# Kernel tuning notes

Measured on AMD Instinct MI355X. Metric: run time of the kernel, lower is better.

Reference implementation:

```python
import jax, jax.numpy as jnp
import numpy as np

B, N, M, D, H, F = 2, 2048, 2048, 512, 8, 2048
EPS = 1e-6


def _ln(x, g, b):
    mu = x.mean(-1, keepdims=True)
    var = ((x - mu) ** 2).mean(-1, keepdims=True)
    return (x - mu) / jnp.sqrt(var + EPS) * g + b


def setup_inputs() -> dict:
    key = jax.random.key(0)
    ks = jax.random.split(key, 12)
    g = lambda k, s: (jax.random.normal(k, s, jnp.float32) * 0.02)
    inp = {
        "x": jax.random.normal(ks[0], (B, N, D), jnp.float32),
        "y": jax.random.normal(ks[1], (B, M, D), jnp.float32),
        "mask_x": jnp.ones((B, N), jnp.float32),
        "mask_y": jnp.ones((B, M), jnp.float32),
        # MaskAttention params (weights stored as [in, out], applied as x @ W + b)
        "Wq": g(ks[2], (D, D)), "bq": jnp.zeros((D,), jnp.float32),
        "Wk": g(ks[3], (D, D)), "bk": jnp.zeros((D,), jnp.float32),
        "Wv": g(ks[4], (D, D)), "bv": jnp.zeros((D,), jnp.float32),
        "Wo": g(ks[5], (D, D)), "bo": jnp.zeros((D,), jnp.float32),
        # Mlp params
        "W1": g(ks[6], (D, F)), "b1": g(ks[7], (F,)) * 1e-4,
        "W2": g(ks[8], (F, D)), "b2": g(ks[9], (D,)) * 1e-4,
        # LayerNorm params (attention_norm shared between x and y; ffn_norm)
        "ln1_g": jnp.ones((D,), jnp.float32), "ln1_b": jnp.zeros((D,), jnp.float32),
        "ln2_g": jnp.ones((D,), jnp.float32), "ln2_b": jnp.zeros((D,), jnp.float32),
    }
    return inp


def reference(x, y, mask_x, mask_y, Wq, bq, Wk, bk, Wv, bv, Wo, bo,
              W1, b1, W2, b2, ln1_g, ln1_b, ln2_g, ln2_b):
    b, n, d = x.shape
    dh = d // H
    h = x
    xn = _ln(x, ln1_g, ln1_b)   # shared attention_norm
    yn = _ln(y, ln1_g, ln1_b)
    # masked Q/K/V projections (mask applied to mixed layers before head split)
    q = (xn @ Wq + bq) * mask_x[..., None]
    k = (yn @ Wk + bk) * mask_y[..., None]
    v = (yn @ Wv + bv) * mask_y[..., None]
    q = q.reshape(b, n, H, dh)
    k = k.reshape(b, -1, H, dh)
    v = v.reshape(b, -1, H, dh)
    scores = jnp.einsum("bnhd,bmhd->bhnm", q, k) / np.sqrt(dh)  # [B,H,N,M]
    probs = jax.nn.softmax(scores, axis=-1)
    ctx = jnp.einsum("bhnm,bmhd->bnhd", probs, v).reshape(b, n, d)
    attn_out = ctx @ Wo + bo  # proj_dropout is identity in eval
    x = h + attn_out
    h2 = x
    xn2 = _ln(x, ln2_g, ln2_b)
    ff = jax.nn.gelu(xn2 @ W1 + b1, approximate=False) @ W2 + b2
    return h2 + ff
```

## Files before the change

kernel.cpp:

```cpp
#include <hip/hip_runtime.h>
#include <hip/hip_bf16.h>

#define B_  2
#define N_  2048
#define M_  2048
#define D_  512
#define H_  8
#define F_  2048
#define DH_ 64
#define ROWS 4096

#define SPLIT 2
#define KV_PER (M_ / SPLIT)
#define NT (KV_PER / 64)
#define ATT_GRID (16 * 16 * SPLIT)

typedef __bf16 bf16x8 __attribute__((ext_vector_type(8)));
typedef __bf16 bf16x4v __attribute__((ext_vector_type(4)));
typedef float  f32x4  __attribute__((ext_vector_type(4)));
using bf16 = __hip_bfloat16;

__global__ __launch_bounds__(256) void ln_kernel(
    const float* __restrict__ in, const float* __restrict__ gam,
    const float* __restrict__ bet, bf16* __restrict__ out)
{
    int wave = threadIdx.x >> 6, lane = threadIdx.x & 63;
    int row  = blockIdx.x * 4 + wave;
    const float* p = in + (size_t)row * D_ + lane * 8;
    float4 v0 = *(const float4*)p;
    float4 v1 = *(const float4*)(p + 4);
    float s  = v0.x + v0.y + v0.z + v0.w + v1.x + v1.y + v1.z + v1.w;
    float ss = v0.x*v0.x + v0.y*v0.y + v0.z*v0.z + v0.w*v0.w
             + v1.x*v1.x + v1.y*v1.y + v1.z*v1.z + v1.w*v1.w;
    for (int m = 1; m < 64; m <<= 1) {
        s  += __shfl_xor(s,  m, 64);
        ss += __shfl_xor(ss, m, 64);
    }
    float mu   = s * (1.f / D_);
    float var  = ss * (1.f / D_) - mu * mu;
    float rstd = rsqrtf(var + 1e-6f);
    int c = lane * 8;
    float4 g0 = *(const float4*)(gam + c), g1 = *(const float4*)(gam + c + 4);
    float4 b0 = *(const float4*)(bet + c), b1 = *(const float4*)(bet + c + 4);
    bf16* o = out + (size_t)row * D_ + c;
    o[0] = __float2bfloat16((v0.x - mu) * rstd * g0.x + b0.x);
    o[1] = __float2bfloat16((v0.y - mu) * rstd * g0.y + b0.y);
    o[2] = __float2bfloat16((v0.z - mu) * rstd * g0.z + b0.z);
    o[3] = __float2bfloat16((v0.w - mu) * rstd * g0.w + b0.w);
    o[4] = __float2bfloat16((v1.x - mu) * rstd * g1.x + b1.x);
    o[5] = __float2bfloat16((v1.y - mu) * rstd * g1.y + b1.y);
    o[6] = __float2bfloat16((v1.z - mu) * rstd * g1.z + b1.z);
    o[7] = __float2bfloat16((v1.w - mu) * rstd * g1.w + b1.w);
}

__global__ void wtrans_kernel(const float* __restrict__ W, bf16* __restrict__ Wt,
                              int K, int N)
{
    __shared__ float t[32][33];
    int tx = threadIdx.x, ty = threadIdx.y;
    int n0 = blockIdx.x * 32, k0 = blockIdx.y * 32;
    for (int j = 0; j < 32; j += 8)
        t[ty + j][tx] = W[(size_t)(k0 + ty + j) * N + n0 + tx];
    __syncthreads();
    for (int j = 0; j < 32; j += 8)
        Wt[(size_t)(n0 + ty + j) * K + k0 + tx] = __float2bfloat16(t[tx][ty + j]);
}

__global__ void wtrans4_kernel(const float* __restrict__ Wq, const float* __restrict__ Wk,
                               const float* __restrict__ Wv, const float* __restrict__ Wo,
                               bf16* __restrict__ Wqt, bf16* __restrict__ Wkt,
                               bf16* __restrict__ Wvt, bf16* __restrict__ Wot)
{
    int z = blockIdx.z;
    const float* W = z == 0 ? Wq : (z == 1 ? Wk : (z == 2 ? Wv : Wo));
    bf16* Wt       = z == 0 ? Wqt : (z == 1 ? Wkt : (z == 2 ? Wvt : Wot));
    __shared__ float t[32][33];
    int tx = threadIdx.x, ty = threadIdx.y;
    int n0 = blockIdx.x * 32, k0 = blockIdx.y * 32;
    for (int j = 0; j < 32; j += 8)
        t[ty + j][tx] = W[(size_t)(k0 + ty + j) * D_ + n0 + tx];
    __syncthreads();
    for (int j = 0; j < 32; j += 8)
        Wt[(size_t)(n0 + ty + j) * D_ + k0 + tx] = __float2bfloat16(t[tx][ty + j]);
}

__global__ void vtrans_kernel(const bf16* __restrict__ v, bf16* __restrict__ vt)
{
    __shared__ bf16 t[32][33];
    int tx = threadIdx.x, ty = threadIdx.y;
    int bh = blockIdx.z, b = bh >> 3, h = bh & 7;
    int m0 = blockIdx.x * 32, d0 = blockIdx.y * 32;
    for (int j = 0; j < 32; j += 8)
        t[ty + j][tx] = v[(size_t)(b * M_ + m0 + ty + j) * D_ + h * DH_ + d0 + tx];
    __syncthreads();
    for (int j = 0; j < 32; j += 8)
        vt[((size_t)bh * DH_ + d0 + ty + j) * M_ + m0 + tx] = t[tx][ty + j];
}

#define BM 128
#define BN 128
#define BK 32
#define LDK 40

#define GEMM_BODY(Aptr, Btptr, KK, EPILOGUE)                                         \
    __shared__ bf16 As[BM * LDK];                                                    \
    __shared__ bf16 Bs[BN * LDK];                                                    \
    int t = threadIdx.x;                                                             \
    int lane = t & 63, wave = t >> 6;                                                \
    int wm = wave >> 1, wn = wave & 1;                                               \
    int r16 = lane & 15, g = lane >> 4;                                              \
    int m0 = blockIdx.x * BM, n0 = blockIdx.y * BN;                                  \
    f32x4 acc[4][4] = {};                                                            \
    for (int k0 = 0; k0 < (KK); k0 += BK) {                                          \
        __syncthreads();                                                             \
        for (int it = 0; it < 2; ++it) {                                             \
            int c = it * 256 + t;                                                    \
            int row = c >> 2, ko = (c & 3) * 8;                                      \
            uint4 dA = *(const uint4*)((Aptr)  + (size_t)(m0 + row) * (KK) + k0 + ko); \
            *(uint4*)((char*)As + row * (LDK * 2) + ko * 2) = dA;                    \
            uint4 dB = *(const uint4*)((Btptr) + (size_t)(n0 + row) * (KK) + k0 + ko); \
            *(uint4*)((char*)Bs + row * (LDK * 2) + ko * 2) = dB;                    \
        }                                                                            \
        __syncthreads();                                                             \
        bf16x8 af[4], bfr[4];                                                        \
        for (int i = 0; i < 4; ++i)                                                  \
            af[i]  = *(const bf16x8*)((char*)As + (wm * 64 + i * 16 + r16) * (LDK * 2) + g * 16); \
        for (int i = 0; i < 4; ++i)                                                  \
            bfr[i] = *(const bf16x8*)((char*)Bs + (wn * 64 + i * 16 + r16) * (LDK * 2) + g * 16); \
        for (int i = 0; i < 4; ++i)                                                  \
            for (int j = 0; j < 4; ++j)                                              \
                acc[i][j] = __builtin_amdgcn_mfma_f32_16x16x32_bf16(af[i], bfr[j], acc[i][j], 0, 0, 0); \
    }                                                                                \
    for (int i = 0; i < 4; ++i) {                                                    \
        int rb = m0 + wm * 64 + i * 16 + g * 4;                                      \
        for (int j = 0; j < 4; ++j) {                                                \
            int cb = n0 + wn * 64 + j * 16 + r16;                                    \
            float bia = bias[cb];                                                    \
            for (int e = 0; e < 4; ++e) {                                            \
                int rr = rb + e;                                                     \
                float val = acc[i][j][e] + bia;                                      \
                EPILOGUE                                                             \
            }                                                                        \
        }                                                                            \
    }

template<bool GELU, bool RESID, bool ROWMASK, bool OUTBF>
__global__ __launch_bounds__(256) void gemm_bt(
    const bf16* __restrict__ A, const bf16* __restrict__ Bt,
    const float* __restrict__ bias, const float* __restrict__ resid,
    const float* __restrict__ rowmask,
    bf16* __restrict__ outb, float* __restrict__ outf,
    int Mr, int Nn, int K)
{
    GEMM_BODY(A, Bt, K,
        if (GELU)    val = 0.5f * val * (1.f + erff(val * 0.70710678118654752f));
        if (RESID)   val += resid[(size_t)rr * Nn + cb];
        if (ROWMASK) val *= rowmask[rr];
        if (OUTBF)   outb[(size_t)rr * Nn + cb] = __float2bfloat16(val);
        else         outf[(size_t)rr * Nn + cb] = val;
    )
}

template<bool RESID, bool ROWMASK, bool OUTBF>
__device__ __forceinline__ void gemm64_body(
    const bf16* __restrict__ A, const bf16* __restrict__ Bt,
    const float* __restrict__ bias, const float* __restrict__ resid,
    const float* __restrict__ rowmask,
    bf16* __restrict__ outb, float* __restrict__ outf,
    int Nn, int K)
{
    __shared__ __align__(16) char As[2][64 * 128];
    __shared__ __align__(16) char Bs[2][64 * 128];
    int t = threadIdx.x, lane = t & 63, wave = t >> 6;
    int wm = wave >> 1, wn = wave & 1;
    int r16 = lane & 15, g = lane >> 4;
    int m0 = blockIdx.x * 64, n0 = blockIdx.y * 64;

    const int sr0 = t >> 3, sr1 = sr0 + 32, sc = t & 7;
    const int wof0 = sr0 * 128 + ((sc ^ (sr0 & 7)) << 4);
    const int wof1 = sr1 * 128 + ((sc ^ (sr1 & 7)) << 4);
    const int rsw0 = ((g     ^ (r16 & 7)) << 4);
    const int rsw1 = (((4 + g) ^ (r16 & 7)) << 4);

    uint4 a0, a1, b0, b1;
#define G64_LOAD(k0)                                                         \
    a0 = *(const uint4*)(A  + (size_t)(m0 + sr0) * K + (k0) + sc * 8);       \
    a1 = *(const uint4*)(A  + (size_t)(m0 + sr1) * K + (k0) + sc * 8);       \
    b0 = *(const uint4*)(Bt + (size_t)(n0 + sr0) * K + (k0) + sc * 8);       \
    b1 = *(const uint4*)(Bt + (size_t)(n0 + sr1) * K + (k0) + sc * 8);
#define G64_WRITE(buf)                                                       \
    *(uint4*)(As[buf] + wof0) = a0;  *(uint4*)(As[buf] + wof1) = a1;         \
    *(uint4*)(Bs[buf] + wof0) = b0;  *(uint4*)(Bs[buf] + wof1) = b1;

    f32x4 acc[2][2] = {};
    G64_LOAD(0)
    G64_WRITE(0)
    int cur = 0;
    const int nit = K >> 6;
    for (int it = 0; it < nit; ++it) {
        if (it + 1 < nit) { G64_LOAD((it + 1) << 6) }
        __syncthreads();
        bf16x8 af[2][2], bfr[2][2];
#pragma unroll
        for (int i = 0; i < 2; ++i) {
            af[i][0] = *(const bf16x8*)(As[cur] + (wm * 32 + i * 16 + r16) * 128 + rsw0);
            af[i][1] = *(const bf16x8*)(As[cur] + (wm * 32 + i * 16 + r16) * 128 + rsw1);
            bfr[i][0] = *(const bf16x8*)(Bs[cur] + (wn * 32 + i * 16 + r16) * 128 + rsw0);
            bfr[i][1] = *(const bf16x8*)(Bs[cur] + (wn * 32 + i * 16 + r16) * 128 + rsw1);
        }
        __builtin_amdgcn_s_setprio(1);
#pragma unroll
        for (int i = 0; i < 2; ++i)
#pragma unroll
            for (int j = 0; j < 2; ++j) {
                acc[i][j] = __builtin_amdgcn_mfma_f32_16x16x32_bf16(af[i][0], bfr[j][0], acc[i][j], 0, 0, 0);
                acc[i][j] = __builtin_amdgcn_mfma_f32_16x16x32_bf16(af[i][1], bfr[j][1], acc[i][j], 0, 0, 0);
            }
        __builtin_amdgcn_s_setprio(0);
        if (it + 1 < nit) { G64_WRITE(cur ^ 1) }
        cur ^= 1;
    }
#undef G64_LOAD
#undef G64_WRITE

#pragma unroll
    for (int i = 0; i < 2; ++i) {
        int rb = m0 + wm * 32 + i * 16 + g * 4;
#pragma unroll
        for (int j = 0; j < 2; ++j) {
            int cb = n0 + wn * 32 + j * 16 + r16;
            float bia = bias[cb];
#pragma unroll
            for (int e = 0; e < 4; ++e) {
                int rr = rb + e;
                float val = acc[i][j][e] + bia;
                if (RESID)   val += resid[(size_t)rr * Nn + cb];
                if (ROWMASK) val *= rowmask[rr];
                if (OUTBF)   outb[(size_t)rr * Nn + cb] = __float2bfloat16(val);
                else         outf[(size_t)rr * Nn + cb] = val;
            }
        }
    }
}

template<bool RESID, bool OUTBF>
__global__ __launch_bounds__(256) void gemm64(
    const bf16* __restrict__ A, const bf16* __restrict__ Bt,
    const float* __restrict__ bias, const float* __restrict__ resid,
    bf16* __restrict__ outb, float* __restrict__ outf, int Nn, int K)
{
    gemm64_body<RESID, false, OUTBF>(A, Bt, bias, resid, nullptr, outb, outf, Nn, K);
}

__global__ __launch_bounds__(256) void gemm64_qkv(
    const bf16* __restrict__ xn, const bf16* __restrict__ yn,
    const bf16* __restrict__ Wqt, const bf16* __restrict__ Wkt, const bf16* __restrict__ Wvt,
    const float* __restrict__ bq, const float* __restrict__ bk, const float* __restrict__ bv,
    const float* __restrict__ mask_x, const float* __restrict__ mask_y,
    bf16* __restrict__ qb, bf16* __restrict__ kb, bf16* __restrict__ vb)
{
    int z = blockIdx.z;
    const bf16* A        = z == 0 ? xn : yn;
    const bf16* Bt       = z == 0 ? Wqt : (z == 1 ? Wkt : Wvt);
    const float* bias    = z == 0 ? bq  : (z == 1 ? bk  : bv);
    const float* rowmask = z == 0 ? mask_x : mask_y;
    bf16* outb           = z == 0 ? qb  : (z == 1 ? kb  : vb);
    gemm64_body<false, true, true>(A, Bt, bias, nullptr, rowmask, outb, nullptr, D_, D_);
}

__global__ __launch_bounds__(256, 3) void attn_kernel(
    const bf16* __restrict__ q, const bf16* __restrict__ kk,
    const bf16* __restrict__ vt, bf16* __restrict__ num,
    float* __restrict__ ml)
{
    int bid = blockIdx.x;
    int wg  = (bid & 7) * (ATT_GRID / 8) + (bid >> 3);
    int n0  = (wg & 15) * 128;
    int bh  = (wg >> 4) & 15;
    int sp  = wg >> 8;
    int b = bh >> 3, h = bh & 7;
    int t = threadIdx.x, lane = t & 63, wave = t >> 6;
    int ql = lane & 15, gg = lane >> 4;

    __shared__ __align__(16) char KsB[2][64 * 128];
    __shared__ __align__(16) char VsB[2][64 * 128];
    __shared__ __align__(16) bf16 plds[4][16][72];

    bf16x8 qf0[2], qf1[2];
    {
        int qr0 = b * N_ + n0 + wave * 32 + ql;
        for (int ks = 0; ks < 2; ++ks) {
            bf16x8 qv = *(const bf16x8*)(q + (size_t)qr0 * D_ + h * DH_ + ks * 32 + gg * 8);
            for (int j = 0; j < 8; ++j) qv[j] = (__bf16)((float)qv[j] * 0.125f);
            qf0[ks] = qv;
            bf16x8 qw = *(const bf16x8*)(q + (size_t)(qr0 + 16) * D_ + h * DH_ + ks * 32 + gg * 8);
            for (int j = 0; j < 8; ++j) qw[j] = (__bf16)((float)qw[j] * 0.125f);
            qf1[ks] = qw;
        }
    }

    f32x4 cacc0[4] = {}, cacc1[4] = {};
    float m0r = -1e30f, l0r = 0.f, m1r = -1e30f, l1r = 0.f;

    const bf16* kbase = kk + (size_t)(b * M_ + sp * KV_PER) * D_ + h * DH_;
    const bf16* vtb   = vt + (size_t)bh * DH_ * M_ + sp * KV_PER;

    const int k0r = t >> 3,          kc0 = t & 7;
    const int k1r = (t >> 3) + 32;
    const int wofs0 = k0r * 128 + ((kc0 ^ (k0r & 7)) << 4);
    const int wofs1 = k1r * 128 + ((kc0 ^ (k1r & 7)) << 4);
    const int rsw0 = ((gg     ^ (ql & 7)) << 4);
    const int rsw1 = (((4 + gg) ^ (ql & 7)) << 4);

#define STAGE_LOAD(tt)                                                              \
    kw0 = *(const uint4*)(kbase + (size_t)((tt) * 64 + k0r) * D_ + kc0 * 8);        \
    kw1 = *(const uint4*)(kbase + (size_t)((tt) * 64 + k1r) * D_ + kc0 * 8);        \
    vw0 = *(const uint4*)(vtb + (size_t)k0r * M_ + (tt) * 64 + kc0 * 8);            \
    vw1 = *(const uint4*)(vtb + (size_t)k1r * M_ + (tt) * 64 + kc0 * 8);

#define STAGE_WRITE(buf)                                                            \
    *(uint4*)(KsB[buf] + wofs0) = kw0;                                              \
    *(uint4*)(KsB[buf] + wofs1) = kw1;                                              \
    *(uint4*)(VsB[buf] + wofs0) = vw0;                                              \
    *(uint4*)(VsB[buf] + wofs1) = vw1;

#define SOFTMAX_PV(S, MR, LR, CACC)                                                 \
    {                                                                               \
        float tmax = fmaxf(                                                         \
            fmaxf(fmaxf(fmaxf(S[0][0], S[0][1]), fmaxf(S[0][2], S[0][3])),          \
                  fmaxf(fmaxf(S[1][0], S[1][1]), fmaxf(S[1][2], S[1][3]))),         \
            fmaxf(fmaxf(fmaxf(S[2][0], S[2][1]), fmaxf(S[2][2], S[2][3])),          \
                  fmaxf(fmaxf(S[3][0], S[3][1]), fmaxf(S[3][2], S[3][3]))));        \
        tmax = fmaxf(tmax, __shfl_xor(tmax, 16, 64));                               \
        tmax = fmaxf(tmax, __shfl_xor(tmax, 32, 64));                               \
        if (__any(tmax - MR > 8.f)) {                     \
            float mnew = fmaxf(MR, tmax);                                           \
            float scl  = __expf(MR - mnew);                                         \
            MR = mnew;                                                              \
            LR *= scl;                                                              \
            for (int df = 0; df < 4; ++df)                                          \
                for (int e = 0; e < 4; ++e) CACC[df][e] *= scl;                     \
        }                                                                           \
        float p[4][4]; float ps = 0.f;                                              \
        for (int nf = 0; nf < 4; ++nf)                                              \
            for (int e = 0; e < 4; ++e) { p[nf][e] = __expf(S[nf][e] - MR); ps += p[nf][e]; } \
        ps += __shfl_xor(ps, 16, 64);                                               \
        ps += __shfl_xor(ps, 32, 64);                                               \
        LR += ps;                                                                   \
        for (int nf = 0; nf < 4; ++nf) {                                            \
            bf16x4v w;                                                              \
            w[0] = (__bf16)p[nf][0]; w[1] = (__bf16)p[nf][1];                       \
            w[2] = (__bf16)p[nf][2]; w[3] = (__bf16)p[nf][3];                       \
            *(bf16x4v*)(&plds[wave][ql][nf * 16 + 4 * gg]) = w;                     \
        }                                                                           \
        __builtin_amdgcn_s_setprio(1);                                              \
        for (int ks = 0; ks < 2; ++ks) {                                            \
            bf16x8 pf = *(const bf16x8*)((const char*)&plds[wave][0][0]             \
                                         + ql * 144 + ks * 64 + gg * 16);           \
            for (int df = 0; df < 4; ++df)                                          \
                CACC[df] = __builtin_amdgcn_mfma_f32_16x16x32_bf16(                 \
                    vf[df * 2 + ks], pf, CACC[df], 0, 0, 0);                        \
        }                                                                           \
        __builtin_amdgcn_s_setprio(0);                                              \
    }

    uint4 kw0, kw1, vw0, vw1;
    STAGE_LOAD(0)
    STAGE_WRITE(0)
    int cur = 0;

    for (int tt = 0; tt < NT; ++tt) {
        if (tt + 1 < NT) { STAGE_LOAD(tt + 1) }
        __syncthreads();

        const char* Kb = KsB[cur];
        const char* Vb = VsB[cur];

        bf16x8 kf[8];
#pragma unroll
        for (int nf = 0; nf < 4; ++nf) {
            kf[nf * 2 + 0] = *(const bf16x8*)(Kb + (nf * 16 + ql) * 128 + rsw0);
            kf[nf * 2 + 1] = *(const bf16x8*)(Kb + (nf * 16 + ql) * 128 + rsw1);
        }

        f32x4 s0[4] = {}, s1[4] = {};
        __builtin_amdgcn_s_setprio(1);
#pragma unroll
        for (int nf = 0; nf < 4; ++nf) {
            s0[nf] = __builtin_amdgcn_mfma_f32_16x16x32_bf16(kf[nf * 2 + 0], qf0[0], s0[nf], 0, 0, 0);
            s0[nf] = __builtin_amdgcn_mfma_f32_16x16x32_bf16(kf[nf * 2 + 1], qf0[1], s0[nf], 0, 0, 0);
            s1[nf] = __builtin_amdgcn_mfma_f32_16x16x32_bf16(kf[nf * 2 + 0], qf1[0], s1[nf], 0, 0, 0);
            s1[nf] = __builtin_amdgcn_mfma_f32_16x16x32_bf16(kf[nf * 2 + 1], qf1[1], s1[nf], 0, 0, 0);
        }
        __builtin_amdgcn_s_setprio(0);

        bf16x8 vf[8];
#pragma unroll
        for (int df = 0; df < 4; ++df) {
            vf[df * 2 + 0] = *(const bf16x8*)(Vb + (df * 16 + ql) * 128 + rsw0);
            vf[df * 2 + 1] = *(const bf16x8*)(Vb + (df * 16 + ql) * 128 + rsw1);
        }

        SOFTMAX_PV(s0, m0r, l0r, cacc0)
        SOFTMAX_PV(s1, m1r, l1r, cacc1)

        if (tt + 1 < NT) { STAGE_WRITE(cur ^ 1) }
        cur ^= 1;
    }

    {
        int qr0 = b * N_ + n0 + wave * 32 + ql;
        bf16* nb0 = num + (size_t)sp * ROWS * D_ + (size_t)qr0 * D_ + h * DH_;
        bf16* nb1 = num + (size_t)sp * ROWS * D_ + (size_t)(qr0 + 16) * D_ + h * DH_;
#pragma unroll
        for (int df = 0; df < 4; ++df) {
            bf16x4v w0, w1;
#pragma unroll
            for (int e = 0; e < 4; ++e) {
                w0[e] = (__bf16)cacc0[df][e];
                w1[e] = (__bf16)cacc1[df][e];
            }
            *(bf16x4v*)(nb0 + df * 16 + 4 * gg) = w0;
            *(bf16x4v*)(nb1 + df * 16 + 4 * gg) = w1;
        }
        if (lane < 16) {
            size_t base = ((size_t)(sp * (B_ * H_) + bh) * N_ + (n0 + wave * 32 + ql)) * 2;
            ml[base] = m0r; ml[base + 1] = l0r;
            size_t base1 = ((size_t)(sp * (B_ * H_) + bh) * N_ + (n0 + wave * 32 + 16 + ql)) * 2;
            ml[base1] = m1r; ml[base1 + 1] = l1r;
        }
    }
#undef STAGE_LOAD
#undef STAGE_WRITE
#undef SOFTMAX_PV
}

__global__ __launch_bounds__(256) void attn_combine(
    const bf16* __restrict__ num, const float* __restrict__ ml,
    bf16* __restrict__ ctx)
{
    int idx = blockIdx.x * 256 + threadIdx.x;
    int row = idx >> 7;
    int c4  = (idx & 127) << 2;
    int b = row >> 11, n = row & (N_ - 1);
    int h = c4 >> 6;
    int bh = (b << 3) + h;
    float mv[SPLIT], lv[SPLIT];
#pragma unroll
    for (int sp = 0; sp < SPLIT; ++sp) {
        const float* mp = ml + ((size_t)(sp * (B_ * H_) + bh) * N_ + n) * 2;
        mv[sp] = mp[0]; lv[sp] = mp[1];
    }
    float mx = mv[0];
#pragma unroll
    for (int sp = 1; sp < SPLIT; ++sp) mx = fmaxf(mx, mv[sp]);
    float den = 0.f;
    float wsc[SPLIT];
#pragma unroll
    for (int sp = 0; sp < SPLIT; ++sp) {
        wsc[sp] = __expf(mv[sp] - mx);
        den += wsc[sp] * lv[sp];
    }
    float inv = 1.f / den;
    float ax = 0.f, ay = 0.f, az = 0.f, aw = 0.f;
#pragma unroll
    for (int sp = 0; sp < SPLIT; ++sp) {
        bf16x4v v = *(const bf16x4v*)(num + (size_t)sp * ROWS * D_ + (size_t)row * D_ + c4);
        ax += wsc[sp] * (float)v[0]; ay += wsc[sp] * (float)v[1];
        az += wsc[sp] * (float)v[2]; aw += wsc[sp] * (float)v[3];
    }
    bf16* o = ctx + (size_t)row * D_ + c4;
    o[0] = __float2bfloat16(ax * inv);
    o[1] = __float2bfloat16(ay * inv);
    o[2] = __float2bfloat16(az * inv);
    o[3] = __float2bfloat16(aw * inv);
}

extern "C" void kernel_launch(void* const* d_in, const int* in_sizes, int n_in,
                              void* d_out, int out_size, void* d_ws, size_t ws_size,
                              hipStream_t stream)
{
    const float* x      = (const float*)d_in[0];
    const float* y      = (const float*)d_in[1];
    const float* mask_x = (const float*)d_in[2];
    const float* mask_y = (const float*)d_in[3];
    const float* Wq = (const float*)d_in[4];  const float* bq = (const float*)d_in[5];
    const float* Wk = (const float*)d_in[6];  const float* bk = (const float*)d_in[7];
    const float* Wv = (const float*)d_in[8];  const float* bv = (const float*)d_in[9];
    const float* Wo = (const float*)d_in[10]; const float* bo = (const float*)d_in[11];
    const float* W1 = (const float*)d_in[12]; const float* b1 = (const float*)d_in[13];
    const float* W2 = (const float*)d_in[14]; const float* b2 = (const float*)d_in[15];
    const float* ln1g = (const float*)d_in[16]; const float* ln1b = (const float*)d_in[17];
    const float* ln2g = (const float*)d_in[18]; const float* ln2b = (const float*)d_in[19];

    char* ws = (char*)d_ws;
    const size_t SZA = (size_t)ROWS * D_ * 2;
    bf16* xn   = (bf16*)ws;            ws += SZA;
    bf16* yn   = (bf16*)ws;            ws += SZA;
    bf16* qb   = (bf16*)ws;            ws += SZA;
    bf16* kb   = (bf16*)ws;            ws += SZA;
    bf16* vb   = (bf16*)ws;            ws += SZA;
    bf16* vtb  = (bf16*)ws;            ws += SZA;
    bf16* ctxb = (bf16*)ws;            ws += SZA;
    bf16* xn2  = (bf16*)ws;            ws += SZA;
    bf16* hff  = (bf16*)ws;            ws += (size_t)ROWS * F_ * 2;
    float* x1  = (float*)ws;           ws += (size_t)ROWS * D_ * 4;
    bf16* Wqt = (bf16*)ws;             ws += (size_t)D_ * D_ * 2;
    bf16* Wkt = (bf16*)ws;             ws += (size_t)D_ * D_ * 2;
    bf16* Wvt = (bf16*)ws;             ws += (size_t)D_ * D_ * 2;
    bf16* Wot = (bf16*)ws;             ws += (size_t)D_ * D_ * 2;
    bf16* W1t = (bf16*)ws;             ws += (size_t)D_ * F_ * 2;
    bf16* W2t = (bf16*)ws;             ws += (size_t)F_ * D_ * 2;
    bf16* numb = (bf16*)ws;            ws += (size_t)SPLIT * ROWS * D_ * 2;
    float* mlb = (float*)ws;           ws += (size_t)SPLIT * B_ * H_ * N_ * 2 * 4;

    dim3 tb(32, 8);
    wtrans4_kernel<<<dim3(D_ / 32, D_ / 32, 4), tb, 0, stream>>>(
        Wq, Wk, Wv, Wo, Wqt, Wkt, Wvt, Wot);
    wtrans_kernel<<<dim3(F_ / 32, D_ / 32), tb, 0, stream>>>(W1, W1t, D_, F_);
    wtrans_kernel<<<dim3(D_ / 32, F_ / 32), tb, 0, stream>>>(W2, W2t, F_, D_);

    ln_kernel<<<ROWS / 4, 256, 0, stream>>>(x, ln1g, ln1b, xn);
    ln_kernel<<<ROWS / 4, 256, 0, stream>>>(y, ln1g, ln1b, yn);

    gemm64_qkv<<<dim3(ROWS / 64, D_ / 64, 3), 256, 0, stream>>>(
        xn, yn, Wqt, Wkt, Wvt, bq, bk, bv, mask_x, mask_y, qb, kb, vb);

    vtrans_kernel<<<dim3(M_ / 32, DH_ / 32, B_ * H_), tb, 0, stream>>>(vb, vtb);

    attn_kernel<<<ATT_GRID, 256, 0, stream>>>(qb, kb, vtb, numb, mlb);
    attn_combine<<<(ROWS * D_ / 4) / 256, 256, 0, stream>>>(numb, mlb, ctxb);

    gemm64<true, false><<<dim3(ROWS / 64, D_ / 64), 256, 0, stream>>>(
        ctxb, Wot, bo, x, nullptr, x1, D_, D_);

    ln_kernel<<<ROWS / 4, 256, 0, stream>>>(x1, ln2g, ln2b, xn2);

    gemm_bt<true, false, false, true><<<dim3(ROWS / BM, F_ / BN), 256, 0, stream>>>(
        xn2, W1t, b1, nullptr, nullptr, hff, nullptr, ROWS, F_, D_);

    gemm64<true, false><<<dim3(ROWS / 64, D_ / 64), 256, 0, stream>>>(
        hff, W2t, b2, x1, nullptr, (float*)d_out, D_, F_);
}
```

Baseline: 126.1 us.

## Fuse LN launches, fold V transpose into QKV epilogue, add pipelined GEMM128

The two first-stage LayerNorm launches become one kernel covering x and y rows. The V projection now writes its output transposed per head directly from the GEMM epilogue, which removes the separate vtrans kernel and the intermediate V buffer. The W1 GELU GEMM moves to a new 128x128 kernel with BK=64, swizzled LDS, register-prefetched double buffering and MFMA priority hints. This trims launch overhead and memory traffic, at the cost of strided 8-byte stores in the V epilogue and higher LDS use in the new GEMM.

```diff
diff --git a/kernel.cpp b/kernel.cpp
--- a/kernel.cpp
+++ b/kernel.cpp
@@ -20,12 +20,18 @@
 typedef float  f32x4  __attribute__((ext_vector_type(4)));
 using bf16 = __hip_bfloat16;
 
-__global__ __launch_bounds__(256) void ln_kernel(
-    const float* __restrict__ in, const float* __restrict__ gam,
-    const float* __restrict__ bet, bf16* __restrict__ out)
+__global__ __launch_bounds__(256) void ln12_kernel(
+    const float* __restrict__ xi, const float* __restrict__ yi,
+    const float* __restrict__ gam, const float* __restrict__ bet,
+    bf16* __restrict__ xo, bf16* __restrict__ yo)
 {
     int wave = threadIdx.x >> 6, lane = threadIdx.x & 63;
-    int row  = blockIdx.x * 4 + wave;
+    int grow = blockIdx.x * 4 + wave;
+    const float* in;
+    bf16* out;
+    int row;
+    if (grow < ROWS) { in = xi; out = xo; row = grow; }
+    else             { in = yi; out = yo; row = grow - ROWS; }
     const float* p = in + (size_t)row * D_ + lane * 8;
     float4 v0 = *(const float4*)p;
     float4 v1 = *(const float4*)(p + 4);
@@ -53,6 +59,39 @@
     o[7] = __float2bfloat16((v1.w - mu) * rstd * g1.w + b1.w);
 }
 
+__global__ __launch_bounds__(256) void ln_kernel(
+    const float* __restrict__ in, const float* __restrict__ gam,
+    const float* __restrict__ bet, bf16* __restrict__ out)
+{
+    int wave = threadIdx.x >> 6, lane = threadIdx.x & 63;
+    int row  = blockIdx.x * 4 + wave;
+    const float* p = in + (size_t)row * D_ + lane * 8;
+    float4 v0 = *(const float4*)p;
+    float4 v1 = *(const float4*)(p + 4);
+    float s  = v0.x + v0.y + v0.z + v0.w + v1.x + v1.y + v1.z + v1.w;
+    float ss = v0.x*v0.x + v0.y*v0.y + v0.z*v0.z + v0.w*v0.w
+             + v1.x*v1.x + v1.y*v1.y + v1.z*v1.z + v1.w*v1.w;
+    for (int m = 1; m < 64; m <<= 1) {
+        s  += __shfl_xor(s,  m, 64);
+        ss += __shfl_xor(ss, m, 64);
+    }
+    float mu   = s * (1.f / D_);
+    float var  = ss * (1.f / D_) - mu * mu;
+    float rstd = rsqrtf(var + 1e-6f);
+    int c = lane * 8;
+    float4 g0 = *(const float4*)(gam + c), g1 = *(const float4*)(gam + c + 4);
+    float4 b0 = *(const float4*)(bet + c), b1 = *(const float4*)(bet + c + 4);
+    bf16* o = out + (size_t)row * D_ + c;
+    o[0] = __float2bfloat16((v0.x - mu) * rstd * g0.x + b0.x);
+    o[1] = __float2bfloat16((v0.y - mu) * rstd * g0.y + b0.y);
+    o[2] = __float2bfloat16((v0.z - mu) * rstd * g0.z + b0.z);
+    o[3] = __float2bfloat16((v0.w - mu) * rstd * g0.w + b0.w);
+    o[4] = __float2bfloat16((v1.x - mu) * rstd * g1.x + b1.x);
+    o[5] = __float2bfloat16((v1.y - mu) * rstd * g1.y + b1.y);
+    o[6] = __float2bfloat16((v1.z - mu) * rstd * g1.z + b1.z);
+    o[7] = __float2bfloat16((v1.w - mu) * rstd * g1.w + b1.w);
+}
+
 __global__ void wtrans_kernel(const float* __restrict__ W, bf16* __restrict__ Wt,
                               int K, int N)
 {
@@ -84,84 +123,7 @@
         Wt[(size_t)(n0 + ty + j) * D_ + k0 + tx] = __float2bfloat16(t[tx][ty + j]);
 }
 
-__global__ void vtrans_kernel(const bf16* __restrict__ v, bf16* __restrict__ vt)
-{
-    __shared__ bf16 t[32][33];
-    int tx = threadIdx.x, ty = threadIdx.y;
-    int bh = blockIdx.z, b = bh >> 3, h = bh & 7;
-    int m0 = blockIdx.x * 32, d0 = blockIdx.y * 32;
-    for (int j = 0; j < 32; j += 8)
-        t[ty + j][tx] = v[(size_t)(b * M_ + m0 + ty + j) * D_ + h * DH_ + d0 + tx];
-    __syncthreads();
-    for (int j = 0; j < 32; j += 8)
-        vt[((size_t)bh * DH_ + d0 + ty + j) * M_ + m0 + tx] = t[tx][ty + j];
-}
-
-#define BM 128
-#define BN 128
-#define BK 32
-#define LDK 40
-
-#define GEMM_BODY(Aptr, Btptr, KK, EPILOGUE)                                         \
-    __shared__ bf16 As[BM * LDK];                                                    \
-    __shared__ bf16 Bs[BN * LDK];                                                    \
-    int t = threadIdx.x;                                                             \
-    int lane = t & 63, wave = t >> 6;                                                \
-    int wm = wave >> 1, wn = wave & 1;                                               \
-    int r16 = lane & 15, g = lane >> 4;                                              \
-    int m0 = blockIdx.x * BM, n0 = blockIdx.y * BN;                                  \
-    f32x4 acc[4][4] = {};                                                            \
-    for (int k0 = 0; k0 < (KK); k0 += BK) {                                          \
-        __syncthreads();                                                             \
-        for (int it = 0; it < 2; ++it) {                                             \
-            int c = it * 256 + t;                                                    \
-            int row = c >> 2, ko = (c & 3) * 8;                                      \
-            uint4 dA = *(const uint4*)((Aptr)  + (size_t)(m0 + row) * (KK) + k0 + ko); \
-            *(uint4*)((char*)As + row * (LDK * 2) + ko * 2) = dA;                    \
-            uint4 dB = *(const uint4*)((Btptr) + (size_t)(n0 + row) * (KK) + k0 + ko); \
-            *(uint4*)((char*)Bs + row * (LDK * 2) + ko * 2) = dB;                    \
-        }                                                                            \
-        __syncthreads();                                                             \
-        bf16x8 af[4], bfr[4];                                                        \
-        for (int i = 0; i < 4; ++i)                                                  \
-            af[i]  = *(const bf16x8*)((char*)As + (wm * 64 + i * 16 + r16) * (LDK * 2) + g * 16); \
-        for (int i = 0; i < 4; ++i)                                                  \
-            bfr[i] = *(const bf16x8*)((char*)Bs + (wn * 64 + i * 16 + r16) * (LDK * 2) + g * 16); \
-        for (int i = 0; i < 4; ++i)                                                  \
-            for (int j = 0; j < 4; ++j)                                              \
-                acc[i][j] = __builtin_amdgcn_mfma_f32_16x16x32_bf16(af[i], bfr[j], acc[i][j], 0, 0, 0); \
-    }                                                                                \
-    for (int i = 0; i < 4; ++i) {                                                    \
-        int rb = m0 + wm * 64 + i * 16 + g * 4;                                      \
-        for (int j = 0; j < 4; ++j) {                                                \
-            int cb = n0 + wn * 64 + j * 16 + r16;                                    \
-            float bia = bias[cb];                                                    \
-            for (int e = 0; e < 4; ++e) {                                            \
-                int rr = rb + e;                                                     \
-                float val = acc[i][j][e] + bia;                                      \
-                EPILOGUE                                                             \
-            }                                                                        \
-        }                                                                            \
-    }
-
-template<bool GELU, bool RESID, bool ROWMASK, bool OUTBF>
-__global__ __launch_bounds__(256) void gemm_bt(
-    const bf16* __restrict__ A, const bf16* __restrict__ Bt,
-    const float* __restrict__ bias, const float* __restrict__ resid,
-    const float* __restrict__ rowmask,
-    bf16* __restrict__ outb, float* __restrict__ outf,
-    int Mr, int Nn, int K)
-{
-    GEMM_BODY(A, Bt, K,
-        if (GELU)    val = 0.5f * val * (1.f + erff(val * 0.70710678118654752f));
-        if (RESID)   val += resid[(size_t)rr * Nn + cb];
-        if (ROWMASK) val *= rowmask[rr];
-        if (OUTBF)   outb[(size_t)rr * Nn + cb] = __float2bfloat16(val);
-        else         outf[(size_t)rr * Nn + cb] = val;
-    )
-}
-
-template<bool RESID, bool ROWMASK, bool OUTBF>
+template<bool RESID, bool ROWMASK, bool OUTBF, bool VTRANS>
 __device__ __forceinline__ void gemm64_body(
     const bf16* __restrict__ A, const bf16* __restrict__ Bt,
     const float* __restrict__ bias, const float* __restrict__ resid,
@@ -230,14 +192,28 @@
         for (int j = 0; j < 2; ++j) {
             int cb = n0 + wn * 32 + j * 16 + r16;
             float bia = bias[cb];
-#pragma unroll
-            for (int e = 0; e < 4; ++e) {
-                int rr = rb + e;
-                float val = acc[i][j][e] + bia;
-                if (RESID)   val += resid[(size_t)rr * Nn + cb];
-                if (ROWMASK) val *= rowmask[rr];
-                if (OUTBF)   outb[(size_t)rr * Nn + cb] = __float2bfloat16(val);
-                else         outf[(size_t)rr * Nn + cb] = val;
+            if (VTRANS) {
+                bf16x4v w;
+#pragma unroll
+                for (int e = 0; e < 4; ++e) {
+                    int rr = rb + e;
+                    float val = acc[i][j][e] + bia;
+                    if (ROWMASK) val *= rowmask[rr];
+                    w[e] = (__bf16)val;
+                }
+                int bb = rb >> 11, m = rb & (M_ - 1);
+                int bh = bb * H_ + (cb >> 6), d = cb & (DH_ - 1);
+                *(bf16x4v*)(outb + ((size_t)bh * DH_ + d) * M_ + m) = w;
+            } else {
+#pragma unroll
+                for (int e = 0; e < 4; ++e) {
+                    int rr = rb + e;
+                    float val = acc[i][j][e] + bia;
+                    if (RESID)   val += resid[(size_t)rr * Nn + cb];
+                    if (ROWMASK) val *= rowmask[rr];
+                    if (OUTBF)   outb[(size_t)rr * Nn + cb] = __float2bfloat16(val);
+                    else         outf[(size_t)rr * Nn + cb] = val;
+                }
             }
         }
     }
@@ -249,7 +225,7 @@
     const float* __restrict__ bias, const float* __restrict__ resid,
     bf16* __restrict__ outb, float* __restrict__ outf, int Nn, int K)
 {
-    gemm64_body<RESID, false, OUTBF>(A, Bt, bias, resid, nullptr, outb, outf, Nn, K);
+    gemm64_body<RESID, false, OUTBF, false>(A, Bt, bias, resid, nullptr, outb, outf, Nn, K);
 }
 
 __global__ __launch_bounds__(256) void gemm64_qkv(
@@ -257,15 +233,99 @@
     const bf16* __restrict__ Wqt, const bf16* __restrict__ Wkt, const bf16* __restrict__ Wvt,
     const float* __restrict__ bq, const float* __restrict__ bk, const float* __restrict__ bv,
     const float* __restrict__ mask_x, const float* __restrict__ mask_y,
-    bf16* __restrict__ qb, bf16* __restrict__ kb, bf16* __restrict__ vb)
+    bf16* __restrict__ qb, bf16* __restrict__ kb, bf16* __restrict__ vtb)
 {
     int z = blockIdx.z;
-    const bf16* A        = z == 0 ? xn : yn;
-    const bf16* Bt       = z == 0 ? Wqt : (z == 1 ? Wkt : Wvt);
-    const float* bias    = z == 0 ? bq  : (z == 1 ? bk  : bv);
-    const float* rowmask = z == 0 ? mask_x : mask_y;
-    bf16* outb           = z == 0 ? qb  : (z == 1 ? kb  : vb);
-    gemm64_body<false, true, true>(A, Bt, bias, nullptr, rowmask, outb, nullptr, D_, D_);
+    if (z == 2) {
+        gemm64_body<false, true, true, true>(yn, Wvt, bv, nullptr, mask_y, vtb, nullptr, D_, D_);
+    } else {
+        const bf16* A        = z == 0 ? xn : yn;
+        const bf16* Bt       = z == 0 ? Wqt : Wkt;
+        const float* bias    = z == 0 ? bq  : bk;
+        const float* rowmask = z == 0 ? mask_x : mask_y;
+        bf16* outb           = z == 0 ? qb  : kb;
+        gemm64_body<false, true, true, false>(A, Bt, bias, nullptr, rowmask, outb, nullptr, D_, D_);
+    }
+}
+
+template<bool GELU>
+__global__ __launch_bounds__(256, 2) void gemm128(
+    const bf16* __restrict__ A, const bf16* __restrict__ Bt,
+    const float* __restrict__ bias, bf16* __restrict__ outb,
+    int Nn, int K)
+{
+    __shared__ __align__(16) char As[2][128 * 128];
+    __shared__ __align__(16) char Bs[2][128 * 128];
+    int t = threadIdx.x, lane = t & 63, wave = t >> 6;
+    int wm = wave >> 1, wn = wave & 1;
+    int r16 = lane & 15, g = lane >> 4;
+    int m0 = blockIdx.x * 128, n0 = blockIdx.y * 128;
+
+    const int sr = t >> 3, sc = t & 7;
+    const int swc = ((sc ^ (sr & 7)) << 4);
+    const int rsw0 = ((g     ^ (r16 & 7)) << 4);
+    const int rsw1 = (((4 + g) ^ (r16 & 7)) << 4);
+
+    uint4 a[4], b[4];
+#define G128_LOAD(k0)                                                          \
+    _Pragma("unroll")                                                          \
+    for (int i = 0; i < 4; ++i) {                                              \
+        a[i] = *(const uint4*)(A  + (size_t)(m0 + sr + 32 * i) * K + (k0) + sc * 8); \
+        b[i] = *(const uint4*)(Bt + (size_t)(n0 + sr + 32 * i) * K + (k0) + sc * 8); \
+    }
+#define G128_WRITE(buf)                                                        \
+    _Pragma("unroll")                                                          \
+    for (int i = 0; i < 4; ++i) {                                              \
+        *(uint4*)(As[buf] + (sr + 32 * i) * 128 + swc) = a[i];                 \
+        *(uint4*)(Bs[buf] + (sr + 32 * i) * 128 + swc) = b[i];                 \
+    }
+
+    f32x4 acc[4][4] = {};
+    G128_LOAD(0)
+    G128_WRITE(0)
+    int cur = 0;
+    const int nit = K >> 6;
+    for (int it = 0; it < nit; ++it) {
+        if (it + 1 < nit) { G128_LOAD((it + 1) << 6) }
+        __syncthreads();
+        bf16x8 af[4][2], bfr[4][2];
+#pragma unroll
+        for (int i = 0; i < 4; ++i) {
+            af[i][0]  = *(const bf16x8*)(As[cur] + (wm * 64 + i * 16 + r16) * 128 + rsw0);
+            af[i][1]  = *(const bf16x8*)(As[cur] + (wm * 64 + i * 16 + r16) * 128 + rsw1);
+            bfr[i][0] = *(const bf16x8*)(Bs[cur] + (wn * 64 + i * 16 + r16) * 128 + rsw0);
+            bfr[i][1] = *(const bf16x8*)(Bs[cur] + (wn * 64 + i * 16 + r16) * 128 + rsw1);
+        }
+        __builtin_amdgcn_s_setprio(1);
+#pragma unroll
+        for (int i = 0; i < 4; ++i)
+#pragma unroll
+            for (int j = 0; j < 4; ++j) {
+                acc[i][j] = __builtin_amdgcn_mfma_f32_16x16x32_bf16(af[i][0], bfr[j][0], acc[i][j], 0, 0, 0);
+                acc[i][j] = __builtin_amdgcn_mfma_f32_16x16x32_bf16(af[i][1], bfr[j][1], acc[i][j], 0, 0, 0);
+            }
+        __builtin_amdgcn_s_setprio(0);
+        if (it + 1 < nit) { G128_WRITE(cur ^ 1) }
+        cur ^= 1;
+    }
+#undef G128_LOAD
+#undef G128_WRITE
+
+#pragma unroll
+    for (int i = 0; i < 4; ++i) {
+        int rb = m0 + wm * 64 + i * 16 + g * 4;
+#pragma unroll
+        for (int j = 0; j < 4; ++j) {
+            int cb = n0 + wn * 64 + j * 16 + r16;
+            float bia = bias[cb];
+#pragma unroll
+            for (int e = 0; e < 4; ++e) {
+                float val = acc[i][j][e] + bia;
+                if (GELU) val = 0.5f * val * (1.f + erff(val * 0.70710678118654752f));
+                outb[(size_t)(rb + e) * Nn + cb] = __float2bfloat16(val);
+            }
+        }
+    }
 }
 
 __global__ __launch_bounds__(256, 3) void attn_kernel(
@@ -333,7 +393,7 @@
                   fmaxf(fmaxf(S[3][0], S[3][1]), fmaxf(S[3][2], S[3][3]))));        \
         tmax = fmaxf(tmax, __shfl_xor(tmax, 16, 64));                               \
         tmax = fmaxf(tmax, __shfl_xor(tmax, 32, 64));                               \
-        if (__any(tmax - MR > 8.f)) {                     \
+        if (__any(tmax - MR > 8.f)) {                                               \
             float mnew = fmaxf(MR, tmax);                                           \
             float scl  = __expf(MR - mnew);                                         \
             MR = mnew;                                                              \
@@ -499,7 +559,6 @@
     bf16* yn   = (bf16*)ws;            ws += SZA;
     bf16* qb   = (bf16*)ws;            ws += SZA;
     bf16* kb   = (bf16*)ws;            ws += SZA;
-    bf16* vb   = (bf16*)ws;            ws += SZA;
     bf16* vtb  = (bf16*)ws;            ws += SZA;
     bf16* ctxb = (bf16*)ws;            ws += SZA;
     bf16* xn2  = (bf16*)ws;            ws += SZA;
@@ -520,13 +579,10 @@
     wtrans_kernel<<<dim3(F_ / 32, D_ / 32), tb, 0, stream>>>(W1, W1t, D_, F_);
     wtrans_kernel<<<dim3(D_ / 32, F_ / 32), tb, 0, stream>>>(W2, W2t, F_, D_);
 
-    ln_kernel<<<ROWS / 4, 256, 0, stream>>>(x, ln1g, ln1b, xn);
-    ln_kernel<<<ROWS / 4, 256, 0, stream>>>(y, ln1g, ln1b, yn);
+    ln12_kernel<<<2 * ROWS / 4, 256, 0, stream>>>(x, y, ln1g, ln1b, xn, yn);
 
     gemm64_qkv<<<dim3(ROWS / 64, D_ / 64, 3), 256, 0, stream>>>(
-        xn, yn, Wqt, Wkt, Wvt, bq, bk, bv, mask_x, mask_y, qb, kb, vb);
-
-    vtrans_kernel<<<dim3(M_ / 32, DH_ / 32, B_ * H_), tb, 0, stream>>>(vb, vtb);
+        xn, yn, Wqt, Wkt, Wvt, bq, bk, bv, mask_x, mask_y, qb, kb, vtb);
 
     attn_kernel<<<ATT_GRID, 256, 0, stream>>>(qb, kb, vtb, numb, mlb);
     attn_combine<<<(ROWS * D_ / 4) / 256, 256, 0, stream>>>(numb, mlb, ctxb);
@@ -536,8 +592,8 @@
 
     ln_kernel<<<ROWS / 4, 256, 0, stream>>>(x1, ln2g, ln2b, xn2);
 
-    gemm_bt<true, false, false, true><<<dim3(ROWS / BM, F_ / BN), 256, 0, stream>>>(
-        xn2, W1t, b1, nullptr, nullptr, hff, nullptr, ROWS, F_, D_);
+    gemm128<true><<<dim3(ROWS / 128, F_ / 128), 256, 0, stream>>>(
+        xn2, W1t, b1, hff, F_, D_);
 
     gemm64<true, false><<<dim3(ROWS / 64, D_ / 64), 256, 0, stream>>>(
         hff, W2t, b2, x1, nullptr, (float*)d_out, D_, F_);
```

Result: slower. 145.8 us (+15.6%).
